# Performance work log

Measured on AMD Instinct MI355X. Metric: run time of the kernel, lower is better.

The kernel has to match this reference:

```python
import jax, jax.numpy as jnp
import numpy as np

B, S, D, H, FF = 2, 2048, 1024, 16, 4096
DH = D // H
EPS = 1e-5


def rmsnorm(x, g):
    rms = jnp.sqrt(jnp.mean(x * x, axis=-1, keepdims=True) + EPS)
    return x / rms * g


def gelu(x):
    return x * 0.5 * (1.0 + jax.lax.erf(x / np.float32(np.sqrt(2.0))))


def setup_inputs() -> dict:
    key = jax.random.key(0)
    ks = jax.random.split(key, 9)
    sd = np.float32(1.0 / np.sqrt(D))
    sf = np.float32(1.0 / np.sqrt(FF))
    return {
        'x': jax.random.normal(ks[0], (B, S, D), jnp.float32),
        'wq': jax.random.normal(ks[1], (D, D), jnp.float32) * sd,
        'wk': jax.random.normal(ks[2], (D, D), jnp.float32) * sd,
        'wv': jax.random.normal(ks[3], (D, D), jnp.float32) * sd,
        'wo': jax.random.normal(ks[4], (D, D), jnp.float32) * sd,
        'w1': jax.random.normal(ks[5], (FF, D), jnp.float32) * sd,
        'w2': jax.random.normal(ks[6], (D, FF), jnp.float32) * sf,
        'g1': jax.random.uniform(ks[7], (D,), jnp.float32),
        'g2': jax.random.uniform(ks[8], (D,), jnp.float32),
    }


def reference(x, wq, wk, wv, wo, w1, w2, g1, g2):
    b, s, d = x.shape
    h = rmsnorm(x, g1)
    # torch Linear: y = x @ W.T ; split heads -> [b, s, H, DH]
    q = jnp.einsum('bsd,ed->bse', h, wq).reshape(b, s, H, DH)
    k = jnp.einsum('bsd,ed->bse', h, wk).reshape(b, s, H, DH)
    v = jnp.einsum('bsd,ed->bse', h, wv).reshape(b, s, H, DH)
    score = jnp.einsum('bqhd,bkhd->bhqk', q, k) / np.float32(np.sqrt(DH))
    causal = jnp.triu(jnp.ones((s, s), bool), 1)  # strictly upper = masked
    score = score + jnp.where(causal, jnp.float32(-1e9), jnp.float32(0.0))
    attn_w = jax.nn.softmax(score, axis=-1)
    o = jnp.einsum('bhqk,bkhd->bqhd', attn_w, v).reshape(b, s, d)
    attn_out = jnp.einsum('bsd,ed->bse', o, wo)
    x2 = attn_out + x
    h2 = rmsnorm(x2, g2)
    ffn = jnp.einsum('bsf,df->bsd', gelu(jnp.einsum('bsd,fd->bsf', h2, w1)), w2)
    return ffn + x2
```

## Files before the change

kernel.cpp:

```cpp
#include <hip/hip_runtime.h>
#include <cstdint>

#define B_ 2
#define S_ 2048
#define D_ 1024
#define H_ 16
#define DH_ 64
#define FF_ 4096
#define M_TOK (B_ * S_)

typedef __attribute__((ext_vector_type(8))) short short8;
typedef __attribute__((ext_vector_type(4))) float f32x4;
typedef __attribute__((ext_vector_type(4))) unsigned short us4;

typedef unsigned short u16;

#define SCL 0.18033688011112042f

__device__ __forceinline__ float bf2f(u16 u) {
  union { uint32_t u; float f; } x;
  x.u = ((uint32_t)u) << 16;
  return x.f;
}
__device__ __forceinline__ u16 f2bf(float f) {
  union { float f; uint32_t u; } x;
  x.f = f;
  uint32_t r = x.u + 0x7FFFu + ((x.u >> 16) & 1u);
  return (u16)(r >> 16);
}

__device__ __forceinline__ void gl_lds16(const void* g, void* l) {
  __builtin_amdgcn_global_load_lds(
      (const __attribute__((address_space(1))) uint32_t*)(uintptr_t)g,
      (__attribute__((address_space(3))) uint32_t*)(uintptr_t)l, 16, 0, 0);
}

__device__ __forceinline__ float gelu_f(float v) {
  const float y = 0.7978845608f * (v + 0.044715f * v * v * v);
  const float t = exp2f(y * 2.885390082f);
  const float th = 1.0f - 2.0f * __builtin_amdgcn_rcpf(t + 1.0f);
  return 0.5f * v * (1.0f + th);
}

#define MEG 1048576
__global__ __launch_bounds__(256) void cvt_all_k(const float* __restrict__ wq, const float* __restrict__ wk,
                                                 const float* __restrict__ wv, const float* __restrict__ wo,
                                                 const float* __restrict__ w1, const float* __restrict__ w2,
                                                 u16* __restrict__ wqkv, u16* __restrict__ wob,
                                                 u16* __restrict__ w1b, u16* __restrict__ w2b) {
  const int n = (blockIdx.x * 256 + threadIdx.x) * 4;
  const float* src;
  u16* dst;
  int off;
  if (n < 3 * MEG) {
    dst = wqkv; off = n;
    src = (n < MEG) ? wq + n : (n < 2 * MEG ? wk + (n - MEG) : wv + (n - 2 * MEG));
  } else if (n < 4 * MEG) {
    dst = wob; off = n - 3 * MEG; src = wo + off;
  } else if (n < 8 * MEG) {
    dst = w1b; off = n - 4 * MEG; src = w1 + off;
  } else {
    dst = w2b; off = n - 8 * MEG; src = w2 + off;
  }
  const float4 v = *(const float4*)src;
  us4 o;
  o[0] = f2bf(v.x); o[1] = f2bf(v.y); o[2] = f2bf(v.z); o[3] = f2bf(v.w);
  *(us4*)&dst[off] = o;
}

__global__ __launch_bounds__(256) void zero_k(float* __restrict__ Of, float* __restrict__ L) {
  const int i = (blockIdx.x * 256 + threadIdx.x) * 4;
  if (i < 4 * MEG) { *(float4*)&Of[i] = float4{0.f, 0.f, 0.f, 0.f}; }
  else { *(float4*)&L[i - 4 * MEG] = float4{0.f, 0.f, 0.f, 0.f}; }
}

__global__ __launch_bounds__(256) void norm_o_k(const float* __restrict__ Of, const float* __restrict__ L,
                                                u16* __restrict__ O) {
  const int row = blockIdx.x;
  const int tid = threadIdx.x;
  const int col = tid * 4;
  const int hh = col >> 6;
  const float lv = L[(size_t)((row >> 11) * 16 + hh) * 2048 + (row & 2047)];
  const float inv = 1.0f / lv;
  const float4 v = *(const float4*)&Of[(size_t)row * D_ + col];
  us4 o;
  o[0] = f2bf(v.x * inv); o[1] = f2bf(v.y * inv);
  o[2] = f2bf(v.z * inv); o[3] = f2bf(v.w * inv);
  *(us4*)&O[(size_t)row * D_ + col] = o;
}

__global__ __launch_bounds__(256) void rmsnorm_k(const float* __restrict__ X,
                                                 const float* __restrict__ G,
                                                 u16* __restrict__ Hout) {
  const int row = blockIdx.x;
  const int tid = threadIdx.x;
  const float4 xx = *(const float4*)&X[(size_t)row * D_ + tid * 4];
  float v[4] = {xx.x, xx.y, xx.z, xx.w};
  float s = 0.f;
#pragma unroll
  for (int i = 0; i < 4; ++i) s += v[i] * v[i];
#pragma unroll
  for (int d = 1; d < 64; d <<= 1) s += __shfl_xor(s, d);
  __shared__ float red[4];
  if ((tid & 63) == 0) red[tid >> 6] = s;
  __syncthreads();
  s = red[0] + red[1] + red[2] + red[3];
  const float scale = rsqrtf(s * (1.0f / (float)D_) + 1e-5f);
  const float4 gg = *(const float4*)&G[tid * 4];
  us4 o;
  o[0] = f2bf(v[0] * scale * gg.x);
  o[1] = f2bf(v[1] * scale * gg.y);
  o[2] = f2bf(v[2] * scale * gg.z);
  o[3] = f2bf(v[3] * scale * gg.w);
  *(us4*)&Hout[(size_t)row * D_ + tid * 4] = o;
}

__global__ __launch_bounds__(256) void rmsnorm_wo_k(const u16* __restrict__ P0, const u16* __restrict__ P1,
                                                    const float* __restrict__ X, const float* __restrict__ G,
                                                    float* __restrict__ X2, u16* __restrict__ Hout) {
  const int row = blockIdx.x;
  const int tid = threadIdx.x;
  const size_t off = (size_t)row * D_ + tid * 4;
  const us4 p0 = *(const us4*)&P0[off];
  const us4 p1 = *(const us4*)&P1[off];
  const float4 xx = *(const float4*)&X[off];
  float v[4];
  v[0] = bf2f(p0[0]) + bf2f(p1[0]) + xx.x;
  v[1] = bf2f(p0[1]) + bf2f(p1[1]) + xx.y;
  v[2] = bf2f(p0[2]) + bf2f(p1[2]) + xx.z;
  v[3] = bf2f(p0[3]) + bf2f(p1[3]) + xx.w;
  *(float4*)&X2[off] = float4{v[0], v[1], v[2], v[3]};
  float s = 0.f;
#pragma unroll
  for (int i = 0; i < 4; ++i) s += v[i] * v[i];
#pragma unroll
  for (int d = 1; d < 64; d <<= 1) s += __shfl_xor(s, d);
  __shared__ float red[4];
  if ((tid & 63) == 0) red[tid >> 6] = s;
  __syncthreads();
  s = red[0] + red[1] + red[2] + red[3];
  const float scale = rsqrtf(s * (1.0f / (float)D_) + 1e-5f);
  const float4 gg = *(const float4*)&G[tid * 4];
  us4 o;
  o[0] = f2bf(v[0] * scale * gg.x);
  o[1] = f2bf(v[1] * scale * gg.y);
  o[2] = f2bf(v[2] * scale * gg.z);
  o[3] = f2bf(v[3] * scale * gg.w);
  *(us4*)&Hout[off] = o;
}

__global__ __launch_bounds__(256) void ffn2_red_k(const u16* __restrict__ Q0, const u16* __restrict__ Q1,
                                                  float* __restrict__ OUT) {
  const int i = (blockIdx.x * 256 + threadIdx.x) * 4;
  const us4 a = *(const us4*)&Q0[i];
  const us4 b = *(const us4*)&Q1[i];
  const float4 c = *(const float4*)&OUT[i];
  *(float4*)&OUT[i] = float4{bf2f(a[0]) + bf2f(b[0]) + c.x, bf2f(a[1]) + bf2f(b[1]) + c.y,
                             bf2f(a[2]) + bf2f(b[2]) + c.z, bf2f(a[3]) + bf2f(b[3]) + c.w};
}

template <int MODE>
__global__ __launch_bounds__(256) void gemm_bt_k(const u16* __restrict__ A,
                                                 const u16* __restrict__ W,
                                                 u16* __restrict__ C0, u16* __restrict__ C1,
                                                 u16* __restrict__ C2, int N, int K) {
  __shared__ alignas(16) u16 As[128 * 32];
  __shared__ alignas(16) u16 Bs[128 * 32];
  const int tid = threadIdx.x;
  const int wv = tid >> 6, lane = tid & 63;
  const int r = lane & 15, quad = lane >> 4;
  const int nx = gridDim.x;
  const int nwg = nx * gridDim.y;
  const int orig = blockIdx.x + nx * blockIdx.y;
  const int id = (orig & 7) * (nwg >> 3) + (orig >> 3);
  const int bn = (id % nx) * 128;
  const int bm = (id / nx) * 128;
  const int row0 = (wv >> 1) * 64, col0 = (wv & 1) * 64;

  f32x4 acc[4][4] = {};

  int srow[2], sg[2];
#pragma unroll
  for (int jj = 0; jj < 2; ++jj) {
    const int c = wv * 128 + jj * 64 + lane;
    srow[jj] = c >> 2;
    sg[jj] = (c & 3) ^ ((srow[jj] >> 1) & 3);
  }

  for (int k0 = 0; k0 < K; k0 += 32) {
#pragma unroll
    for (int jj = 0; jj < 2; ++jj) {
      const int l0 = (wv * 128 + jj * 64) * 8;
      gl_lds16(&A[(size_t)(bm + srow[jj]) * K + k0 + sg[jj] * 8], &As[l0]);
      gl_lds16(&W[(size_t)(bn + srow[jj]) * K + k0 + sg[jj] * 8], &Bs[l0]);
    }
    __syncthreads();
    short8 af[4], bf[4];
#pragma unroll
    for (int mt = 0; mt < 4; ++mt) {
      const int mr = row0 + mt * 16 + r;
      af[mt] = *(const short8*)&As[mr * 32 + (quad ^ ((mr >> 1) & 3)) * 8];
    }
#pragma unroll
    for (int nt = 0; nt < 4; ++nt) {
      const int nr = col0 + nt * 16 + r;
      bf[nt] = *(const short8*)&Bs[nr * 32 + (quad ^ ((nr >> 1) & 3)) * 8];
    }
#pragma unroll
    for (int mt = 0; mt < 4; ++mt)
#pragma unroll
      for (int nt = 0; nt < 4; ++nt)
        acc[mt][nt] = __builtin_amdgcn_mfma_f32_16x16x32_bf16(af[mt], bf[nt], acc[mt][nt], 0, 0, 0);
    __syncthreads();
  }

  if constexpr (MODE == 2) {
#pragma unroll
    for (int mt = 0; mt < 4; ++mt)
#pragma unroll
      for (int nt = 0; nt < 4; ++nt)
#pragma unroll
        for (int i = 0; i < 4; ++i) {
          const int grow = bm + row0 + mt * 16 + quad * 4 + i;
          const int gcol = bn + col0 + nt * 16 + r;
          C0[(size_t)grow * N + gcol] = f2bf(gelu_f(acc[mt][nt][i]));
        }
  } else {
#pragma unroll
    for (int mt = 0; mt < 4; ++mt) {
      const int grow0 = bm + row0 + mt * 16 + quad * 4;
#pragma unroll
      for (int nt = 0; nt < 4; ++nt) {
        const int gcol = bn + col0 + nt * 16 + r;
        if (gcol < 2048) {
          u16* dst = (gcol < 1024) ? C0 : C1;
          const float sc = (gcol < 1024) ? SCL : 1.0f;
          const int cc = gcol & 1023;
#pragma unroll
          for (int i = 0; i < 4; ++i)
            dst[(size_t)(grow0 + i) * 1024 + cc] = f2bf(acc[mt][nt][i] * sc);
        } else {
          const int vcol = gcol - 2048;
          us4 o;
#pragma unroll
          for (int i = 0; i < 4; ++i) o[i] = f2bf(acc[mt][nt][i]);
          const size_t addr =
              ((size_t)((grow0 >> 11) * 16 + (vcol >> 6)) * 64 + (vcol & 63)) * 2048 + (grow0 & 2047);
          *(us4*)&C2[addr] = o;
        }
      }
    }
  }
}

__global__ __launch_bounds__(256) void gemm_sk2_k(const u16* __restrict__ A,
                                                  const u16* __restrict__ W,
                                                  u16* __restrict__ P0, u16* __restrict__ P1,
                                                  int N, int K, int KS) {
  __shared__ alignas(16) u16 As[128 * 32];
  __shared__ alignas(16) u16 Bs[128 * 32];
  const int tid = threadIdx.x;
  const int wv = tid >> 6, lane = tid & 63;
  const int r = lane & 15, quad = lane >> 4;
  const int orig = blockIdx.x + 8 * (blockIdx.y + 32 * blockIdx.z);
  const int id = (orig & 7) * 64 + (orig >> 3);
  const int bn = (id & 7) * 128;
  const int bm = ((id >> 3) & 31) * 128;
  const int bz = id >> 8;
  const int row0 = (wv >> 1) * 64, col0 = (wv & 1) * 64;
  const int koff = bz * KS;
  u16* P = bz ? P1 : P0;

  f32x4 acc[4][4] = {};

  int srow[2], sg[2];
#pragma unroll
  for (int jj = 0; jj < 2; ++jj) {
    const int c = wv * 128 + jj * 64 + lane;
    srow[jj] = c >> 2;
    sg[jj] = (c & 3) ^ ((srow[jj] >> 1) & 3);
  }

  for (int k0 = koff; k0 < koff + KS; k0 += 32) {
#pragma unroll
    for (int jj = 0; jj < 2; ++jj) {
      const int l0 = (wv * 128 + jj * 64) * 8;
      gl_lds16(&A[(size_t)(bm + srow[jj]) * K + k0 + sg[jj] * 8], &As[l0]);
      gl_lds16(&W[(size_t)(bn + srow[jj]) * K + k0 + sg[jj] * 8], &Bs[l0]);
    }
    __syncthreads();
    short8 af[4], bf[4];
#pragma unroll
    for (int mt = 0; mt < 4; ++mt) {
      const int mr = row0 + mt * 16 + r;
      af[mt] = *(const short8*)&As[mr * 32 + (quad ^ ((mr >> 1) & 3)) * 8];
    }
#pragma unroll
    for (int nt = 0; nt < 4; ++nt) {
      const int nr = col0 + nt * 16 + r;
      bf[nt] = *(const short8*)&Bs[nr * 32 + (quad ^ ((nr >> 1) & 3)) * 8];
    }
#pragma unroll
    for (int mt = 0; mt < 4; ++mt)
#pragma unroll
      for (int nt = 0; nt < 4; ++nt)
        acc[mt][nt] = __builtin_amdgcn_mfma_f32_16x16x32_bf16(af[mt], bf[nt], acc[mt][nt], 0, 0, 0);
    __syncthreads();
  }

#pragma unroll
  for (int mt = 0; mt < 4; ++mt)
#pragma unroll
    for (int nt = 0; nt < 4; ++nt)
#pragma unroll
      for (int i = 0; i < 4; ++i) {
        const int grow = bm + row0 + mt * 16 + quad * 4 + i;
        const int gcol = bn + col0 + nt * 16 + r;
        P[(size_t)grow * N + gcol] = f2bf(acc[mt][nt][i]);
      }
}

__global__ __launch_bounds__(256, 2) void attn_k(const u16* __restrict__ Q,
                                                 const u16* __restrict__ Kx,
                                                 const u16* __restrict__ VT,
                                                 float* __restrict__ Of, float* __restrict__ L) {
  __shared__ alignas(16) u16 Ks[2][32 * 72];
  __shared__ alignas(16) u16 Vs[2][64 * 40];
  __shared__ alignas(16) u16 Ps[4][32 * 40];

  const int tid = threadIdx.x;
  const int wv = tid >> 6, lane = tid & 63;
  const int r = lane & 15, quad = lane >> 4;

  const int orig = blockIdx.x + 40 * blockIdx.y;
  const int sid = (orig & 7) * 160 + (orig >> 3);
  const int sx = sid % 40;
  const int bh = sid / 40;
  const int b = bh >> 4, hh = bh & 15;

  int id = 39 - sx;
  int bx = 0;
  for (;;) {
    const int nb = (bx >> 2) + 1;
    if (id < nb) break;
    id -= nb;
    ++bx;
  }
  const int c = id;
  const int j0base = c * 512;
  const int niter = (min(bx * 128 + 128, j0base + 512) - j0base) >> 5;

  const int qbase = bx * 128;
  const int m0 = qbase + wv * 32;
  const size_t base = (size_t)b * S_ * D_ + (size_t)hh * DH_;
  const u16* Qb = Q + base;
  const u16* Kb = Kx + base;
  const u16* VTb = VT + (size_t)bh * 64 * 2048;
  u16* Psw = &Ps[wv][0];

  short8 qf[2][2];
#pragma unroll
  for (int f = 0; f < 2; ++f) {
    qf[f][0] = *(const short8*)&Qb[(size_t)(m0 + f * 16 + r) * D_ + quad * 8];
    qf[f][1] = *(const short8*)&Qb[(size_t)(m0 + f * 16 + r) * D_ + 32 + quad * 8];
  }

  short8 onesv;
#pragma unroll
  for (int e = 0; e < 8; ++e) onesv[e] = (short)0x3F80;

  f32x4 oacc[2][4] = {};
  f32x4 lacc[2] = {};

  const int krow = tid >> 3, kg = tid & 7;
  const int vrow = tid >> 2, vg = tid & 3;

  *(short8*)&Ks[0][krow * 72 + kg * 8] = *(const short8*)&Kb[(size_t)(j0base + krow) * D_ + kg * 8];
  *(short8*)&Vs[0][vrow * 40 + vg * 8] = *(const short8*)&VTb[(size_t)vrow * 2048 + j0base + vg * 8];

  int cur = 0;
  for (int it = 0; it < niter; ++it) {
    const int j0 = j0base + it * 32;
    __syncthreads();

    if (it + 1 < niter) {
      const int j1 = j0 + 32;
      *(short8*)&Ks[cur ^ 1][krow * 72 + kg * 8] =
          *(const short8*)&Kb[(size_t)(j1 + krow) * D_ + kg * 8];
      *(short8*)&Vs[cur ^ 1][vrow * 40 + vg * 8] =
          *(const short8*)&VTb[(size_t)vrow * 2048 + j1 + vg * 8];
    }

    f32x4 z[2][2];
    __builtin_amdgcn_s_setprio(1);
#pragma unroll
    for (int kt = 0; kt < 2; ++kt) {
      const short8 kf0 = *(const short8*)&Ks[cur][(kt * 16 + r) * 72 + quad * 8];
      const short8 kf1 = *(const short8*)&Ks[cur][(kt * 16 + r) * 72 + 32 + quad * 8];
#pragma unroll
      for (int f = 0; f < 2; ++f) {
        f32x4 zz = {};
        zz = __builtin_amdgcn_mfma_f32_16x16x32_bf16(qf[f][0], kf0, zz, 0, 0, 0);
        zz = __builtin_amdgcn_mfma_f32_16x16x32_bf16(qf[f][1], kf1, zz, 0, 0, 0);
        z[f][kt] = zz;
      }
    }
    __builtin_amdgcn_s_setprio(0);

    const bool masked = (j0 + 31 > m0);
#pragma unroll
    for (int f = 0; f < 2; ++f)
#pragma unroll
      for (int i = 0; i < 4; ++i) {
        const int qrow = m0 + f * 16 + quad * 4 + i;
        float v0 = z[f][0][i];
        float v1 = z[f][1][i];
        if (masked) {
          if (j0 + r > qrow) v0 = -128.f;
          if (j0 + 16 + r > qrow) v1 = -128.f;
        }
        const uint32_t pk = (uint32_t)f2bf(exp2f(v0)) | ((uint32_t)f2bf(exp2f(v1)) << 16);
        *(uint32_t*)&Psw[(f * 16 + quad * 4 + i) * 40 + r * 2] = pk;
      }

    asm volatile("s_waitcnt lgkmcnt(0)" ::: "memory");

    short8 vf[4];
#pragma unroll
    for (int nt = 0; nt < 4; ++nt) {
      const us4 va = *(const us4*)&Vs[cur][(nt * 16 + r) * 40 + quad * 4];
      const us4 vb = *(const us4*)&Vs[cur][(nt * 16 + r) * 40 + 16 + quad * 4];
      short8 o;
      o[0] = va[0]; o[1] = vb[0]; o[2] = va[1]; o[3] = vb[1];
      o[4] = va[2]; o[5] = vb[2]; o[6] = va[3]; o[7] = vb[3];
      vf[nt] = o;
    }
    __builtin_amdgcn_s_setprio(1);
#pragma unroll
    for (int f = 0; f < 2; ++f) {
      const short8 pf = *(const short8*)&Psw[(f * 16 + r) * 40 + quad * 8];
#pragma unroll
      for (int nt = 0; nt < 4; ++nt)
        oacc[f][nt] = __builtin_amdgcn_mfma_f32_16x16x32_bf16(pf, vf[nt], oacc[f][nt], 0, 0, 0);
      lacc[f] = __builtin_amdgcn_mfma_f32_16x16x32_bf16(pf, onesv, lacc[f], 0, 0, 0);
    }
    __builtin_amdgcn_s_setprio(0);

    cur ^= 1;
  }

#pragma unroll
  for (int f = 0; f < 2; ++f) {
#pragma unroll
    for (int i = 0; i < 4; ++i) {
      const int qrow = m0 + f * 16 + quad * 4 + i;
#pragma unroll
      for (int nt = 0; nt < 4; ++nt)
        atomicAdd(&Of[base + (size_t)qrow * D_ + nt * 16 + r], oacc[f][nt][i]);
      if (r == 0) atomicAdd(&L[(size_t)bh * 2048 + qrow], lacc[f][i]);
    }
  }
}

extern "C" void kernel_launch(void* const* d_in, const int* in_sizes, int n_in,
                              void* d_out, int out_size, void* d_ws, size_t ws_size,
                              hipStream_t stream) {
  (void)in_sizes; (void)n_in; (void)out_size; (void)ws_size;
  const float* x   = (const float*)d_in[0];
  const float* wq  = (const float*)d_in[1];
  const float* wk  = (const float*)d_in[2];
  const float* wvp = (const float*)d_in[3];
  const float* wo  = (const float*)d_in[4];
  const float* w1  = (const float*)d_in[5];
  const float* w2  = (const float*)d_in[6];
  const float* g1  = (const float*)d_in[7];
  const float* g2  = (const float*)d_in[8];
  float* out = (float*)d_out;

  u16* ws = (u16*)d_ws;
  const size_t TD = (size_t)M_TOK * D_;
  u16* h    = ws;
  u16* q    = ws + 1 * TD;
  u16* k    = ws + 2 * TD;
  u16* vt   = ws + 3 * TD;
  u16* h2   = ws + 4 * TD;
  float* l  = (float*)(ws + 4 * TD);
  u16* o    = h;
  u16* t    = ws;
  u16* P0   = q;
  u16* P1   = k;
  u16* Q0   = h2;
  u16* wqkv = ws + 5 * TD;
  u16* wob  = wqkv + 3 * MEG;
  u16* w1b  = wob + 1 * MEG;
  u16* w2b  = w1b + 4 * MEG;
  u16* Q1   = w2b + 4 * MEG;

  const dim3 blk(256);

  cvt_all_k<<<12288, blk, 0, stream>>>(wq, wk, wvp, wo, w1, w2, wqkv, wob, w1b, w2b);
  zero_k<<<(4 * MEG + 65536) / 1024, blk, 0, stream>>>(out, l);
  rmsnorm_k<<<M_TOK, blk, 0, stream>>>(x, g1, h);
  gemm_bt_k<4><<<dim3(24, 32), blk, 0, stream>>>(h, wqkv, q, k, vt, 3072, 1024);
  attn_k<<<dim3(40, 32), blk, 0, stream>>>(q, k, vt, out, l);
  norm_o_k<<<M_TOK, blk, 0, stream>>>(out, l, o);
  gemm_sk2_k<<<dim3(8, 32, 2), blk, 0, stream>>>(o, wob, P0, P1, 1024, 1024, 512);
  rmsnorm_wo_k<<<M_TOK, blk, 0, stream>>>(P0, P1, x, g2, out, h2);
  gemm_bt_k<2><<<dim3(32, 32), blk, 0, stream>>>(h2, w1b, t, nullptr, nullptr, 4096, 1024);
  gemm_sk2_k<<<dim3(8, 32, 2), blk, 0, stream>>>(t, w2b, Q0, Q1, 1024, 4096, 2048);
  ffn2_red_k<<<4096, blk, 0, stream>>>(Q0, Q1, out);
}
```

Measured before the change: 379.7 us.

## Pre-interleave V^T layout in QKV epilogue and defer K/V LDS stores

The QKV GEMM epilogue now writes V^T in a pre-permuted, pair-interleaved order so the attention kernel can load each V fragment with one 16-byte LDS read instead of two 8-byte reads plus a register shuffle. The attention loop also loads the next K/V tile into registers first and writes it to LDS only after the MFMAs, so global-load latency is hidden behind compute. The epilogue branch is hoisted to a per-block test. This couples two kernels through a nonstandard layout, which adds correctness risk and more register pressure.

```diff
diff --git a/kernel.cpp b/kernel.cpp
--- a/kernel.cpp
+++ b/kernel.cpp
@@ -226,27 +226,36 @@
           C0[(size_t)grow * N + gcol] = f2bf(gelu_f(acc[mt][nt][i]));
         }
   } else {
-#pragma unroll
-    for (int mt = 0; mt < 4; ++mt) {
-      const int grow0 = bm + row0 + mt * 16 + quad * 4;
-#pragma unroll
-      for (int nt = 0; nt < 4; ++nt) {
-        const int gcol = bn + col0 + nt * 16 + r;
-        if (gcol < 2048) {
+    if (bn < 2048) {
+#pragma unroll
+      for (int mt = 0; mt < 4; ++mt) {
+        const int grow0 = bm + row0 + mt * 16 + quad * 4;
+#pragma unroll
+        for (int nt = 0; nt < 4; ++nt) {
+          const int gcol = bn + col0 + nt * 16 + r;
           u16* dst = (gcol < 1024) ? C0 : C1;
           const float sc = (gcol < 1024) ? SCL : 1.0f;
           const int cc = gcol & 1023;
 #pragma unroll
           for (int i = 0; i < 4; ++i)
             dst[(size_t)(grow0 + i) * 1024 + cc] = f2bf(acc[mt][nt][i] * sc);
-        } else {
-          const int vcol = gcol - 2048;
-          us4 o;
-#pragma unroll
-          for (int i = 0; i < 4; ++i) o[i] = f2bf(acc[mt][nt][i]);
-          const size_t addr =
-              ((size_t)((grow0 >> 11) * 16 + (vcol >> 6)) * 64 + (vcol & 63)) * 2048 + (grow0 & 2047);
-          *(us4*)&C2[addr] = o;
+        }
+      }
+    } else {
+#pragma unroll
+      for (int mtp = 0; mtp < 4; mtp += 2) {
+        const int tok0 = bm + row0 + mtp * 16 + quad * 4;
+#pragma unroll
+        for (int nt = 0; nt < 4; ++nt) {
+          const int vcol = bn + col0 + nt * 16 + r - 2048;
+          const size_t vtrow = (size_t)((tok0 >> 11) * 16 + (vcol >> 6)) * 64 + (vcol & 63);
+#pragma unroll
+          for (int i = 0; i < 4; ++i) {
+            const int s = (tok0 + i) & 2047;
+            const uint32_t pk =
+                (uint32_t)f2bf(acc[mtp][nt][i]) | ((uint32_t)f2bf(acc[mtp + 1][nt][i]) << 16);
+            *(uint32_t*)&C2[vtrow * 2048 + s + (s & 15)] = pk;
+          }
         }
       }
     }
@@ -383,12 +392,12 @@
     const int j0 = j0base + it * 32;
     __syncthreads();
 
-    if (it + 1 < niter) {
+    short8 kreg, vreg;
+    const bool pf_next = (it + 1 < niter);
+    if (pf_next) {
       const int j1 = j0 + 32;
-      *(short8*)&Ks[cur ^ 1][krow * 72 + kg * 8] =
-          *(const short8*)&Kb[(size_t)(j1 + krow) * D_ + kg * 8];
-      *(short8*)&Vs[cur ^ 1][vrow * 40 + vg * 8] =
-          *(const short8*)&VTb[(size_t)vrow * 2048 + j1 + vg * 8];
+      kreg = *(const short8*)&Kb[(size_t)(j1 + krow) * D_ + kg * 8];
+      vreg = *(const short8*)&VTb[(size_t)vrow * 2048 + j1 + vg * 8];
     }
 
     f32x4 z[2][2];
@@ -427,14 +436,8 @@
 
     short8 vf[4];
 #pragma unroll
-    for (int nt = 0; nt < 4; ++nt) {
-      const us4 va = *(const us4*)&Vs[cur][(nt * 16 + r) * 40 + quad * 4];
-      const us4 vb = *(const us4*)&Vs[cur][(nt * 16 + r) * 40 + 16 + quad * 4];
-      short8 o;
-      o[0] = va[0]; o[1] = vb[0]; o[2] = va[1]; o[3] = vb[1];
-      o[4] = va[2]; o[5] = vb[2]; o[6] = va[3]; o[7] = vb[3];
-      vf[nt] = o;
-    }
+    for (int nt = 0; nt < 4; ++nt)
+      vf[nt] = *(const short8*)&Vs[cur][(nt * 16 + r) * 40 + quad * 8];
     __builtin_amdgcn_s_setprio(1);
 #pragma unroll
     for (int f = 0; f < 2; ++f) {
@@ -445,6 +448,11 @@
       lacc[f] = __builtin_amdgcn_mfma_f32_16x16x32_bf16(pf, onesv, lacc[f], 0, 0, 0);
     }
     __builtin_amdgcn_s_setprio(0);
+
+    if (pf_next) {
+      *(short8*)&Ks[cur ^ 1][krow * 72 + kg * 8] = kreg;
+      *(short8*)&Vs[cur ^ 1][vrow * 40 + vg * 8] = vreg;
+    }
 
     cur ^= 1;
   }
```

Result: no change. 374.2 us (-1.5%).
